# Kernel tuning notes

Measured on AMD Instinct MI355X. Metric: run time of the kernel, lower is better.

The kernel has to match this reference:

```python
import jax, jax.numpy as jnp
import numpy as np

DIM = 1024
NUM_HEADS = 16
HEAD_DIM = DIM // NUM_HEADS
SCALE = HEAD_DIM ** -0.5


def setup_inputs() -> dict:
    key = jax.random.key(0)
    ks = jax.random.split(key, 9)
    s = DIM ** -0.5
    return {
        'x_q': jax.random.normal(ks[0], (4, 2048, DIM), dtype=jnp.float32),
        'wq': jax.random.normal(ks[1], (DIM, DIM), dtype=jnp.float32) * s,
        'bq': jax.random.normal(ks[2], (DIM,), dtype=jnp.float32) * 0.02,
        'wk': jax.random.normal(ks[3], (DIM, DIM), dtype=jnp.float32) * s,
        'bk': jax.random.normal(ks[4], (DIM,), dtype=jnp.float32) * 0.02,
        'wv': jax.random.normal(ks[5], (DIM, DIM), dtype=jnp.float32) * s,
        'bv': jax.random.normal(ks[6], (DIM,), dtype=jnp.float32) * 0.02,
        'wo': jax.random.normal(ks[7], (DIM, DIM), dtype=jnp.float32) * s,
        'bo': jax.random.normal(ks[8], (DIM,), dtype=jnp.float32) * 0.02,
    }


def reference(x_q, wq, bq, wk, bk, wv, bv, wo, bo):
    B, N, C = x_q.shape
    H, c = NUM_HEADS, HEAD_DIM
    # torch nn.Linear: y = x @ W.T + b, W is [out, in]
    q = (x_q @ wq.T + bq).reshape(B, N, H, c).transpose(0, 2, 1, 3)  # [B,H,N,c]
    k = (x_q @ wk.T + bk).reshape(B, N, H, c).transpose(0, 2, 1, 3)
    v = (x_q @ wv.T + bv).reshape(B, N, H, c).transpose(0, 2, 1, 3)
    attn = jnp.einsum('bhqc,bhkc->bhqk', q, k) * SCALE  # [B,H,N,N]
    attn = jax.nn.softmax(attn, axis=-1)
    out = jnp.einsum('bhqk,bhkc->bhqc', attn, v)  # [B,H,N,c]
    out = out.transpose(0, 2, 1, 3).reshape(B, N, C)
    return out @ wo.T + bo
```

## Files before the change

### kernel.cpp

```cpp
#include <hip/hip_runtime.h>
#include <hip/hip_bf16.h>

typedef __bf16 bf16x8 __attribute__((ext_vector_type(8)));
typedef float f32x4 __attribute__((ext_vector_type(4)));
typedef unsigned int u32x4 __attribute__((ext_vector_type(4)));

#define QSCALE 0.18033688011112042f

__device__ __forceinline__ void gload16(const void* g, void* l) {
  __builtin_amdgcn_global_load_lds(
      (const __attribute__((address_space(1))) uint32_t*)g,
      (__attribute__((address_space(3))) uint32_t*)l, 16, 0, 0);
}

__device__ __forceinline__ unsigned bf16bits(float f) {
  union { __bf16 h; unsigned short u; } c; c.h = (__bf16)f; return c.u;
}

__device__ __forceinline__ float exp2_raw(float x) {
  float r;
  asm("v_exp_f32 %0, %1" : "=v"(r) : "v"(x));
  return r;
}

__device__ __forceinline__ unsigned cvt_pk_bf16(float a, float b) {
  unsigned r;
  asm("v_cvt_pk_bf16_f32 %0, %1, %2" : "=v"(r) : "v"(a), "v"(b));
  return r;
}

#define SWAPL32(a, b) asm("v_permlane32_swap_b32 %0, %1" : "+v"(a), "+v"(b))
#define SWAPL16(a, b) asm("v_permlane16_swap_b32 %0, %1" : "+v"(a), "+v"(b))

__global__ __launch_bounds__(256) void cast_all(
    const float* __restrict__ x, const float* __restrict__ wq, const float* __restrict__ wk,
    const float* __restrict__ wv, const float* __restrict__ wo,
    __bf16* __restrict__ xbf, __bf16* __restrict__ wqb, __bf16* __restrict__ wkb,
    __bf16* __restrict__ wvb, __bf16* __restrict__ wob) {
  int b = blockIdx.x;
  const float* src;
  __bf16* dst;
  int i;
  if (b < 4096) {
    src = x; dst = xbf; i = b * 256 + threadIdx.x;
  } else {
    int s = (b - 4096) >> 9;
    i = ((b - 4096) & 511) * 256 + threadIdx.x;
    src = (s == 0) ? wq : (s == 1) ? wk : (s == 2) ? wv : wo;
    dst = (s == 0) ? wqb : (s == 1) ? wkb : (s == 2) ? wvb : wob;
  }
  const float4* p = (const float4*)src;
  float4 a = p[2 * i], c = p[2 * i + 1];
  bf16x8 v;
  v[0] = (__bf16)a.x; v[1] = (__bf16)a.y; v[2] = (__bf16)a.z; v[3] = (__bf16)a.w;
  v[4] = (__bf16)c.x; v[5] = (__bf16)c.y; v[6] = (__bf16)c.z; v[7] = (__bf16)c.w;
  ((bf16x8*)dst)[i] = v;
}

template <int MODE>
__global__ __launch_bounds__(256) void gemm_nt(
    const __bf16* __restrict__ A,
    const __bf16* __restrict__ W0, const __bf16* __restrict__ W1, const __bf16* __restrict__ W2,
    const float* __restrict__ b0, const float* __restrict__ b1, const float* __restrict__ b2,
    __bf16* __restrict__ o0, __bf16* __restrict__ o1, __bf16* __restrict__ o2,
    float* __restrict__ of) {
  __shared__ __bf16 lA[128 * 32];
  __shared__ __bf16 lB[128 * 32];
  const int t = threadIdx.x;
  const int lane = t & 63;
  const int w = t >> 6;
  const int wr = w >> 1, wc = w & 1;
  const int l16 = lane & 15, l4 = lane >> 4;
  const int m0 = blockIdx.x * 128;
  int sel, bn;
  if (MODE == 0) { sel = blockIdx.y >> 3; bn = (blockIdx.y & 7) * 128; }
  else           { sel = 0;               bn = blockIdx.y * 128; }
  const __bf16* W   = (sel == 0) ? W0 : (sel == 1) ? W1 : W2;
  const float* bias = (sel == 0) ? b0 : (sel == 1) ? b1 : b2;

  f32x4 acc[4][4] = {};

  for (int k0 = 0; k0 < 1024; k0 += 32) {
    __syncthreads();
#pragma unroll
    for (int i = 0; i < 2; i++) {
      int c = t + i * 256;
      int r = c >> 2, cp = c & 3;
      gload16(A + (size_t)(m0 + r) * 1024 + k0 + cp * 8, lA + c * 8);
      gload16(W + (size_t)(bn + r) * 1024 + k0 + cp * 8, lB + c * 8);
    }
    __syncthreads();
    bf16x8 af[4], bfr[4];
#pragma unroll
    for (int m = 0; m < 4; m++)
      af[m] = *(const bf16x8*)(lA + (wr * 64 + m * 16 + l16) * 32 + l4 * 8);
#pragma unroll
    for (int n = 0; n < 4; n++)
      bfr[n] = *(const bf16x8*)(lB + (wc * 64 + n * 16 + l16) * 32 + l4 * 8);
#pragma unroll
    for (int m = 0; m < 4; m++)
#pragma unroll
      for (int n = 0; n < 4; n++)
        acc[m][n] = __builtin_amdgcn_mfma_f32_16x16x32_bf16(af[m], bfr[n], acc[m][n], 0, 0, 0);
  }

  const float scl = (MODE == 0 && sel == 0) ? QSCALE : 1.0f;
  __bf16* outp = (sel == 0) ? o0 : (sel == 1) ? o1 : o2;
#pragma unroll
  for (int n = 0; n < 4; n++) {
    const int col = bn + wc * 64 + n * 16 + l16;
    const float bv = bias[col];
    if (MODE == 0 && sel == 2) {
      const int h = col >> 6, hc = col & 63;
#pragma unroll
      for (int m = 0; m < 4; m++) {
        const int nnb = m0 + wr * 64 + m * 16 + l4 * 4;
        const int b_ = nnb >> 11, nn = nnb & 2047;
        ushort4 ov;
        ov.x = (unsigned short)bf16bits(acc[m][n][0] + bv);
        ov.y = (unsigned short)bf16bits(acc[m][n][1] + bv);
        ov.z = (unsigned short)bf16bits(acc[m][n][2] + bv);
        ov.w = (unsigned short)bf16bits(acc[m][n][3] + bv);
        *(ushort4*)(outp + ((size_t)(b_ * 16 + h) * 64 + hc) * 2048 + nn) = ov;
      }
    } else {
#pragma unroll
      for (int m = 0; m < 4; m++) {
#pragma unroll
        for (int j = 0; j < 4; j++) {
          const int row = m0 + wr * 64 + m * 16 + l4 * 4 + j;
          float v = acc[m][n][j] + bv;
          if (MODE == 0) {
            v *= scl;
            int b_ = row >> 11, nn = row & 2047;
            int h = col >> 6, hc = col & 63;
            outp[(((size_t)(b_ * 16 + h)) * 2048 + nn) * 64 + hc] = (__bf16)v;
          } else {
            of[(size_t)row * 1024 + col] = v;
          }
        }
      }
    }
  }
}

__global__ __launch_bounds__(256) void attn_fwd(const __bf16* __restrict__ Q,
                                                const __bf16* __restrict__ K,
                                                const __bf16* __restrict__ Vt,
                                                __bf16* __restrict__ O) {
  __shared__ __bf16 sm[16384];
  const int flat = blockIdx.x;
  const int wg = (flat & 7) * 128 + (flat >> 3);
  const int bh = wg >> 4;
  const int q0 = (wg & 15) * 128;
  const __bf16* Qh = Q + (size_t)bh * 2048 * 64;
  const __bf16* Kh = K + (size_t)bh * 2048 * 64;
  const __bf16* Vh = Vt + (size_t)bh * 64 * 2048;
  const int t = threadIdx.x, lane = t & 63, w = t >> 6;
  const int l16 = lane & 15, l4 = lane >> 4;

  bf16x8 qf[2][2];
#pragma unroll
  for (int st = 0; st < 2; st++)
#pragma unroll
    for (int kk = 0; kk < 2; kk++)
      qf[st][kk] = *(const bf16x8*)(Qh + (size_t)(q0 + w * 32 + st * 16 + l16) * 64 + kk * 32 + l4 * 8);

  f32x4 ao[2][4] = {};
  f32x4 rs4[2] = {};
  bf16x8 onesf;
#pragma unroll
  for (int i = 0; i < 8; i++) onesf[i] = (__bf16)1.0f;

  const int rdbase = l4 * 512 + l16 * 8;
  const int vb = 8192 + l4 * 512 + l16 * 8;

#pragma unroll
  for (int i = 0; i < 2; i++) {
    int ic = w * 2 + i;
    gload16(Kh + (size_t)lane * 64 + ic * 8, sm + ic * 512 + lane * 8);
    gload16(Vh + (size_t)lane * 2048 + ic * 8, sm + 8192 + ic * 512 + lane * 8);
  }
  __syncthreads();

#define ATTN_STEP(CUR, TNEXT)                                                         \
  {                                                                                   \
    const __bf16* lds = sm + (CUR) * 4096;                                            \
    if ((TNEXT) < 32) {                                                               \
      const int kvn = (TNEXT) * 64;                                                   \
      __bf16* dst = sm + ((CUR) ^ 1) * 4096;                                          \
      _Pragma("unroll")                                                               \
      for (int i = 0; i < 2; i++) {                                                   \
        int ic = w * 2 + i;                                                           \
        gload16(Kh + (size_t)(kvn + lane) * 64 + ic * 8, dst + ic * 512 + lane * 8);  \
        gload16(Vh + (size_t)lane * 2048 + kvn + ic * 8, dst + 8192 + ic * 512 + lane * 8); \
      }                                                                               \
    }                                                                                 \
    f32x4 s[2][4] = {};                                                               \
    __builtin_amdgcn_s_setprio(1);                                                    \
    _Pragma("unroll")                                                                 \
    for (int kk = 0; kk < 2; kk++) {                                                  \
      _Pragma("unroll")                                                               \
      for (int n = 0; n < 4; n++) {                                                   \
        bf16x8 kf = *(const bf16x8*)(lds + rdbase + kk * 2048 + n * 128);             \
        _Pragma("unroll")                                                             \
        for (int st = 0; st < 2; st++)                                                \
          s[st][n] = __builtin_amdgcn_mfma_f32_16x16x32_bf16(kf, qf[st][kk], s[st][n], 0, 0, 0); \
      }                                                                               \
    }                                                                                 \
    __builtin_amdgcn_s_setprio(0);                                                    \
    bf16x8 vf[2][4];                                                                  \
    _Pragma("unroll")                                                                 \
    for (int g = 0; g < 2; g++)                                                       \
      _Pragma("unroll")                                                               \
      for (int cb = 0; cb < 4; cb++)                                                  \
        vf[g][cb] = *(const bf16x8*)(lds + vb + g * 2048 + cb * 128);                 \
    u32x4 pk[2][2];                                                                   \
    _Pragma("unroll")                                                                 \
    for (int st = 0; st < 2; st++) {                                                  \
      _Pragma("unroll")                                                               \
      for (int g = 0; g < 2; g++) {                                                   \
        float p0 = exp2_raw(s[st][2 * g][0]),     p1 = exp2_raw(s[st][2 * g][1]);     \
        float p2 = exp2_raw(s[st][2 * g][2]),     p3 = exp2_raw(s[st][2 * g][3]);     \
        float p4 = exp2_raw(s[st][2 * g + 1][0]), p5 = exp2_raw(s[st][2 * g + 1][1]); \
        float p6 = exp2_raw(s[st][2 * g + 1][2]), p7 = exp2_raw(s[st][2 * g + 1][3]); \
        unsigned c00 = cvt_pk_bf16(p0, p1), c01 = cvt_pk_bf16(p2, p3);                \
        unsigned c10 = cvt_pk_bf16(p4, p5), c11 = cvt_pk_bf16(p6, p7);                \
        SWAPL32(c00, c10); SWAPL32(c01, c11);                                         \
        SWAPL16(c00, c10); SWAPL16(c01, c11);                                         \
        u32x4 tv = {c00, c01, c10, c11};                                              \
        pk[st][g] = tv;                                                               \
      }                                                                               \
    }                                                                                 \
    __builtin_amdgcn_s_setprio(1);                                                    \
    _Pragma("unroll")                                                                 \
    for (int st = 0; st < 2; st++) {                                                  \
      _Pragma("unroll")                                                               \
      for (int g = 0; g < 2; g++) {                                                   \
        union { u32x4 u; bf16x8 h; } cv; cv.u = pk[st][g];                            \
        rs4[st] = __builtin_amdgcn_mfma_f32_16x16x32_bf16(onesf, cv.h, rs4[st], 0, 0, 0); \
        _Pragma("unroll")                                                             \
        for (int cb = 0; cb < 4; cb++)                                                \
          ao[st][cb] = __builtin_amdgcn_mfma_f32_16x16x32_bf16(vf[g][cb], cv.h, ao[st][cb], 0, 0, 0); \
      }                                                                               \
    }                                                                                 \
    __builtin_amdgcn_s_setprio(0);                                                    \
    __syncthreads();                                                                  \
  }

  for (int tkv = 0; tkv < 32; tkv += 2) {
    ATTN_STEP(0, tkv + 1);
    ATTN_STEP(1, tkv + 2);
  }
#undef ATTN_STEP

  const int b_ = bh >> 4, h = bh & 15;
#pragma unroll
  for (int st = 0; st < 2; st++) {
    const float inv = 1.f / rs4[st][0];
    const int qrow = q0 + w * 32 + st * 16 + l16;
#pragma unroll
    for (int cb = 0; cb < 4; cb++) {
      ushort4 ov;
      ov.x = (unsigned short)bf16bits(ao[st][cb][0] * inv);
      ov.y = (unsigned short)bf16bits(ao[st][cb][1] * inv);
      ov.z = (unsigned short)bf16bits(ao[st][cb][2] * inv);
      ov.w = (unsigned short)bf16bits(ao[st][cb][3] * inv);
      *(ushort4*)(O + ((size_t)b_ * 2048 + qrow) * 1024 + h * 64 + cb * 16 + l4 * 4) = ov;
    }
  }
}

extern "C" void kernel_launch(void* const* d_in, const int* in_sizes, int n_in,
                              void* d_out, int out_size, void* d_ws, size_t ws_size,
                              hipStream_t stream) {
  const float* x  = (const float*)d_in[0];
  const float* wq = (const float*)d_in[1];
  const float* bq = (const float*)d_in[2];
  const float* wk = (const float*)d_in[3];
  const float* bk = (const float*)d_in[4];
  const float* wv = (const float*)d_in[5];
  const float* bv = (const float*)d_in[6];
  const float* wo = (const float*)d_in[7];
  const float* bo = (const float*)d_in[8];
  float* out = (float*)d_out;

  const size_t NX = 8388608;
  const size_t NW = 1048576;
  __bf16* xbf = (__bf16*)d_ws;
  __bf16* wqb = xbf + NX;
  __bf16* wkb = wqb + NW;
  __bf16* wvb = wkb + NW;
  __bf16* wob = wvb + NW;
  __bf16* Qb  = wob + NW;
  __bf16* Kb  = Qb + NX;
  __bf16* Vtb = Kb + NX;

  cast_all<<<6144, 256, 0, stream>>>(x, wq, wk, wv, wo, xbf, wqb, wkb, wvb, wob);

  gemm_nt<0><<<dim3(64, 24), 256, 0, stream>>>(xbf, wqb, wkb, wvb, bq, bk, bv,
                                               Qb, Kb, Vtb, nullptr);
  attn_fwd<<<1024, 256, 0, stream>>>(Qb, Kb, Vtb, xbf );
  gemm_nt<1><<<dim3(64, 8), 256, 0, stream>>>(xbf, wob, nullptr, nullptr, bo, nullptr, nullptr,
                                              nullptr, nullptr, nullptr, out);
}
```

Measured before the change: 191.7 us.

## Software-pipeline attention loop: overlap next tile's QK MFMA with current softmax

Restructures the flash-attention inner loop so the QK^T MFMAs for tile T+1 are interleaved with the exp2/pack softmax work of tile T. Two score register sets alternate between iterations, two K/V tiles are prefetched at the start, and the single barrier per step moves to after the V fragment reads. The aim is to hide the transcendental and permute latency behind matrix-core work. In exchange it raises VGPR pressure, which could lower occupancy.

```diff
diff --git a/kernel.cpp b/kernel.cpp
--- a/kernel.cpp
+++ b/kernel.cpp
@@ -175,84 +175,99 @@
   const int rdbase = l4 * 512 + l16 * 8;
   const int vb = 8192 + l4 * 512 + l16 * 8;
 
+  f32x4 sA[2][4], sB[2][4];
+
 #pragma unroll
   for (int i = 0; i < 2; i++) {
     int ic = w * 2 + i;
-    gload16(Kh + (size_t)lane * 64 + ic * 8, sm + ic * 512 + lane * 8);
-    gload16(Vh + (size_t)lane * 2048 + ic * 8, sm + 8192 + ic * 512 + lane * 8);
+    gload16(Kh + (size_t)lane * 64 + ic * 8,          sm + ic * 512 + lane * 8);
+    gload16(Vh + (size_t)lane * 2048 + ic * 8,        sm + 8192 + ic * 512 + lane * 8);
+    gload16(Kh + (size_t)(64 + lane) * 64 + ic * 8,   sm + 4096 + ic * 512 + lane * 8);
+    gload16(Vh + (size_t)lane * 2048 + 64 + ic * 8,   sm + 12288 + ic * 512 + lane * 8);
   }
   __syncthreads();
 
-#define ATTN_STEP(CUR, TNEXT)                                                         \
-  {                                                                                   \
-    const __bf16* lds = sm + (CUR) * 4096;                                            \
-    if ((TNEXT) < 32) {                                                               \
-      const int kvn = (TNEXT) * 64;                                                   \
-      __bf16* dst = sm + ((CUR) ^ 1) * 4096;                                          \
-      _Pragma("unroll")                                                               \
-      for (int i = 0; i < 2; i++) {                                                   \
-        int ic = w * 2 + i;                                                           \
-        gload16(Kh + (size_t)(kvn + lane) * 64 + ic * 8, dst + ic * 512 + lane * 8);  \
+#define QK_N(KLDS, SCUR, n)                                                    \
+  {                                                                            \
+    bf16x8 kf0 = *(const bf16x8*)((KLDS) + rdbase + (n) * 128);                \
+    bf16x8 kf1 = *(const bf16x8*)((KLDS) + rdbase + 2048 + (n) * 128);         \
+    f32x4 z = {};                                                              \
+    SCUR[0][(n)] = __builtin_amdgcn_mfma_f32_16x16x32_bf16(kf0, qf[0][0], z, 0, 0, 0); \
+    SCUR[1][(n)] = __builtin_amdgcn_mfma_f32_16x16x32_bf16(kf0, qf[1][0], z, 0, 0, 0); \
+    SCUR[0][(n)] = __builtin_amdgcn_mfma_f32_16x16x32_bf16(kf1, qf[0][1], SCUR[0][(n)], 0, 0, 0); \
+    SCUR[1][(n)] = __builtin_amdgcn_mfma_f32_16x16x32_bf16(kf1, qf[1][1], SCUR[1][(n)], 0, 0, 0); \
+  }
+
+#define SM_GROUP(SP, st_, g_)                                                  \
+  {                                                                            \
+    float p0 = exp2_raw(SP[(st_)][2 * (g_)][0]),     p1 = exp2_raw(SP[(st_)][2 * (g_)][1]); \
+    float p2 = exp2_raw(SP[(st_)][2 * (g_)][2]),     p3 = exp2_raw(SP[(st_)][2 * (g_)][3]); \
+    float p4 = exp2_raw(SP[(st_)][2 * (g_) + 1][0]), p5 = exp2_raw(SP[(st_)][2 * (g_) + 1][1]); \
+    float p6 = exp2_raw(SP[(st_)][2 * (g_) + 1][2]), p7 = exp2_raw(SP[(st_)][2 * (g_) + 1][3]); \
+    unsigned c00 = cvt_pk_bf16(p0, p1), c01 = cvt_pk_bf16(p2, p3);             \
+    unsigned c10 = cvt_pk_bf16(p4, p5), c11 = cvt_pk_bf16(p6, p7);             \
+    SWAPL32(c00, c10); SWAPL32(c01, c11);                                      \
+    SWAPL16(c00, c10); SWAPL16(c01, c11);                                      \
+    u32x4 tv = {c00, c01, c10, c11};                                           \
+    pk[(st_)][(g_)] = tv;                                                      \
+  }
+
+#define ATTN_ITER(T, CUR, SPREV, SCUR)                                         \
+  {                                                                            \
+    const __bf16* vlds = sm + (CUR) * 4096;                                    \
+    bf16x8 vf[2][4];                                                           \
+    _Pragma("unroll")                                                          \
+    for (int g = 0; g < 2; g++)                                                \
+      _Pragma("unroll")                                                        \
+      for (int cb = 0; cb < 4; cb++)                                           \
+        vf[g][cb] = *(const bf16x8*)(vlds + vb + g * 2048 + cb * 128);         \
+    __syncthreads();                                                           \
+    if ((T) + 2 < 32) {                                                        \
+      const int kvn = ((T) + 2) * 64;                                          \
+      __bf16* dst = sm + (CUR) * 4096;                                         \
+      _Pragma("unroll")                                                        \
+      for (int i = 0; i < 2; i++) {                                            \
+        int ic = w * 2 + i;                                                    \
+        gload16(Kh + (size_t)(kvn + lane) * 64 + ic * 8, dst + ic * 512 + lane * 8); \
         gload16(Vh + (size_t)lane * 2048 + kvn + ic * 8, dst + 8192 + ic * 512 + lane * 8); \
-      }                                                                               \
-    }                                                                                 \
-    f32x4 s[2][4] = {};                                                               \
-    __builtin_amdgcn_s_setprio(1);                                                    \
-    _Pragma("unroll")                                                                 \
-    for (int kk = 0; kk < 2; kk++) {                                                  \
-      _Pragma("unroll")                                                               \
-      for (int n = 0; n < 4; n++) {                                                   \
-        bf16x8 kf = *(const bf16x8*)(lds + rdbase + kk * 2048 + n * 128);             \
-        _Pragma("unroll")                                                             \
-        for (int st = 0; st < 2; st++)                                                \
-          s[st][n] = __builtin_amdgcn_mfma_f32_16x16x32_bf16(kf, qf[st][kk], s[st][n], 0, 0, 0); \
-      }                                                                               \
-    }                                                                                 \
-    __builtin_amdgcn_s_setprio(0);                                                    \
-    bf16x8 vf[2][4];                                                                  \
-    _Pragma("unroll")                                                                 \
-    for (int g = 0; g < 2; g++)                                                       \
-      _Pragma("unroll")                                                               \
-      for (int cb = 0; cb < 4; cb++)                                                  \
-        vf[g][cb] = *(const bf16x8*)(lds + vb + g * 2048 + cb * 128);                 \
-    u32x4 pk[2][2];                                                                   \
-    _Pragma("unroll")                                                                 \
-    for (int st = 0; st < 2; st++) {                                                  \
-      _Pragma("unroll")                                                               \
-      for (int g = 0; g < 2; g++) {                                                   \
-        float p0 = exp2_raw(s[st][2 * g][0]),     p1 = exp2_raw(s[st][2 * g][1]);     \
-        float p2 = exp2_raw(s[st][2 * g][2]),     p3 = exp2_raw(s[st][2 * g][3]);     \
-        float p4 = exp2_raw(s[st][2 * g + 1][0]), p5 = exp2_raw(s[st][2 * g + 1][1]); \
-        float p6 = exp2_raw(s[st][2 * g + 1][2]), p7 = exp2_raw(s[st][2 * g + 1][3]); \
-        unsigned c00 = cvt_pk_bf16(p0, p1), c01 = cvt_pk_bf16(p2, p3);                \
-        unsigned c10 = cvt_pk_bf16(p4, p5), c11 = cvt_pk_bf16(p6, p7);                \
-        SWAPL32(c00, c10); SWAPL32(c01, c11);                                         \
-        SWAPL16(c00, c10); SWAPL16(c01, c11);                                         \
-        u32x4 tv = {c00, c01, c10, c11};                                              \
-        pk[st][g] = tv;                                                               \
-      }                                                                               \
-    }                                                                                 \
-    __builtin_amdgcn_s_setprio(1);                                                    \
-    _Pragma("unroll")                                                                 \
-    for (int st = 0; st < 2; st++) {                                                  \
-      _Pragma("unroll")                                                               \
-      for (int g = 0; g < 2; g++) {                                                   \
-        union { u32x4 u; bf16x8 h; } cv; cv.u = pk[st][g];                            \
+      }                                                                        \
+    }                                                                          \
+    u32x4 pk[2][2];                                                            \
+    __builtin_amdgcn_s_setprio(1);                                             \
+    if ((T) + 1 < 32) {                                                        \
+      const __bf16* klds = sm + ((CUR) ^ 1) * 4096;                            \
+      _Pragma("unroll")                                                        \
+      for (int n = 0; n < 4; n++) {                                            \
+        QK_N(klds, SCUR, n);                                                   \
+        SM_GROUP(SPREV, (n >> 1), (n & 1));                                    \
+      }                                                                        \
+    } else {                                                                   \
+      _Pragma("unroll")                                                        \
+      for (int n = 0; n < 4; n++) SM_GROUP(SPREV, (n >> 1), (n & 1));          \
+    }                                                                          \
+    _Pragma("unroll")                                                          \
+    for (int st = 0; st < 2; st++)                                             \
+      _Pragma("unroll")                                                        \
+      for (int g = 0; g < 2; g++) {                                            \
+        union { u32x4 u; bf16x8 h; } cv; cv.u = pk[st][g];                     \
         rs4[st] = __builtin_amdgcn_mfma_f32_16x16x32_bf16(onesf, cv.h, rs4[st], 0, 0, 0); \
-        _Pragma("unroll")                                                             \
-        for (int cb = 0; cb < 4; cb++)                                                \
+        _Pragma("unroll")                                                      \
+        for (int cb = 0; cb < 4; cb++)                                         \
           ao[st][cb] = __builtin_amdgcn_mfma_f32_16x16x32_bf16(vf[g][cb], cv.h, ao[st][cb], 0, 0, 0); \
-      }                                                                               \
-    }                                                                                 \
-    __builtin_amdgcn_s_setprio(0);                                                    \
-    __syncthreads();                                                                  \
-  }
+      }                                                                        \
+    __builtin_amdgcn_s_setprio(0);                                             \
+  }
+
+#pragma unroll
+  for (int n = 0; n < 4; n++) QK_N(sm, sA, n);
 
   for (int tkv = 0; tkv < 32; tkv += 2) {
-    ATTN_STEP(0, tkv + 1);
-    ATTN_STEP(1, tkv + 2);
-  }
-#undef ATTN_STEP
+    ATTN_ITER(tkv,     0, sA, sB);
+    ATTN_ITER(tkv + 1, 1, sB, sA);
+  }
+#undef ATTN_ITER
+#undef SM_GROUP
+#undef QK_N
 
   const int b_ = bh >> 4, h = bh & 15;
 #pragma unroll
```

Result: faster. 185.3 us (median of 3 runs) (-3.3%).
